# Kernel tuning notes

Hardware: AMD Instinct MI355X
Metric: run time of the kernel (lower is better)

The kernel has to match this reference:

```python
import jax, jax.numpy as jnp
import numpy as np

B, S, T, H, V = 32, 64, 64, 512, 32000


def setup_inputs() -> dict:
    key = jax.random.key(0)
    ks = jax.random.split(key, 16)
    sc = 1.0 / np.sqrt(H)
    return {
        "encoder_outputs": jax.random.normal(ks[0], (B, S, H), jnp.float32),
        "encoder_hidden": jax.random.normal(ks[1], (1, B, H), jnp.float32),
        "target_tensor": jax.random.randint(ks[2], (B, T), 0, V),
        "max_len": T,
        "emb": jax.random.normal(ks[3], (V, H), jnp.float32) * 0.02,
        "Wa_w": jax.random.normal(ks[4], (H, H), jnp.float32) * sc,
        "Wa_b": jnp.zeros((H,), jnp.float32),
        "Ua_w": jax.random.normal(ks[5], (H, H), jnp.float32) * sc,
        "Ua_b": jnp.zeros((H,), jnp.float32),
        "Va_w": jax.random.normal(ks[6], (1, H), jnp.float32) * sc,
        "Va_b": jnp.zeros((1,), jnp.float32),
        "W_ih": jax.random.normal(ks[7], (3 * H, 2 * H), jnp.float32) * sc,
        "W_hh": jax.random.normal(ks[8], (3 * H, H), jnp.float32) * sc,
        "b_ih": jnp.zeros((3 * H,), jnp.float32),
        "b_hh": jnp.zeros((3 * H,), jnp.float32),
        "out_w": jax.random.normal(ks[9], (V, H), jnp.float32) * sc,
        "out_b": jnp.zeros((V,), jnp.float32),
    }


def reference(encoder_outputs, encoder_hidden, target_tensor, max_len,
              emb, Wa_w, Wa_b, Ua_w, Ua_b, Va_w, Va_b,
              W_ih, W_hh, b_ih, b_hh, out_w, out_b):
    # Teacher-forcing decode; dropout in eval mode (identity).
    keys = encoder_outputs                      # [B,S,H]
    Ua_keys = keys @ Ua_w.T + Ua_b              # precompute Ua(keys): same math each step
    bsz = keys.shape[0]
    # token fed at step 0 is SOS (=0), then target_tensor[:, i-1]
    tokens = jnp.concatenate(
        [jnp.zeros((bsz, 1), target_tensor.dtype), target_tensor[:, : max_len - 1]], axis=1
    )  # [B,T]

    def step(h, tok):                            # h: [B,H], tok: [B]
        e = emb[tok]                             # [B,H] embedding gather
        q = h @ Wa_w.T + Wa_b                    # Wa(query)
        s = jnp.tanh(q[:, None, :] + Ua_keys)    # [B,S,H]
        scores = (s @ Va_w.T + Va_b)[..., 0]     # [B,S]
        w = jax.nn.softmax(scores, axis=-1)      # [B,S]
        ctx = jnp.einsum('bs,bsh->bh', w, keys)  # [B,H]
        x = jnp.concatenate([e, ctx], axis=-1)   # [B,2H]
        gi = x @ W_ih.T + b_ih                   # [B,3H]
        gh = h @ W_hh.T + b_hh                   # [B,3H]
        ir, iz, inn = jnp.split(gi, 3, axis=-1)
        hr, hz, hn = jnp.split(gh, 3, axis=-1)
        r = jax.nn.sigmoid(ir + hr)
        z = jax.nn.sigmoid(iz + hz)
        n = jnp.tanh(inn + r * hn)
        h_new = (1.0 - z) * n + z * h            # GRU cell (PyTorch convention)
        logits = h_new @ out_w.T + out_b         # [B,V]
        return h_new, (logits, w)

    h0 = encoder_hidden[0]                       # [B,H]
    hT, (logits, attn) = jax.lax.scan(step, h0, jnp.swapaxes(tokens, 0, 1))
    logits = jnp.swapaxes(logits, 0, 1)          # [B,T,V]
    decoder_outputs = jax.nn.log_softmax(logits, axis=-1)
    attentions = jnp.swapaxes(attn, 0, 1)        # [B,T,S]
    return decoder_outputs, hT[None], attentions
```

## Files before the change

### kernel.cpp

```cpp
#include <hip/hip_runtime.h>
#include <hip/hip_bf16.h>
#include <hip/hip_fp16.h>
#include <math.h>

constexpr int B = 32, S = 64, T = 64, H = 512, V = 32000;
constexpr int G3 = 3 * H;
constexpr int BT = B * T;

constexpr size_t UAK_OFF    = 0;
constexpr size_t GIE_OFF    = 1048576;
constexpr size_t KWTH_OFF   = 4194304;
constexpr size_t WA2T_OFF   = 5767168;
constexpr size_t WHH2T_OFF  = 5898240;
constexpr size_t SCPT_OFF   = 6291456;
constexpr size_t FLG_OFF    = 7340032;
constexpr size_t OWBF_OFF   = 0;
constexpr size_t HALL_OFF   = 8192000;
constexpr size_t STATS_OFF  = 8192000;
constexpr size_t HBF_OFF    = 9256960;
constexpr size_t KEYSH_OFF  = 10000000;
constexpr size_t GEH_OFF    = 10524288;
constexpr size_t UAWH_OFF   = 11048576;
constexpr size_t WLOH_OFF   = 11179648;
constexpr size_t WCTXH_OFF  = 11572864;

typedef __attribute__((ext_vector_type(8))) short bf16x8;
typedef __attribute__((ext_vector_type(4))) float f32x4;
typedef __attribute__((ext_vector_type(4))) int i32x4;
typedef _Float16 f16x8 __attribute__((ext_vector_type(8)));
typedef _Float16 h2v __attribute__((ext_vector_type(2)));

__device__ __forceinline__ float fast_tanh(float x) {
  float ax = fabsf(x);
  float e = __expf(-2.f * ax);
  float r = (1.f - e) / (1.f + e);
  return x < 0.f ? -r : r;
}
__device__ __forceinline__ float fast_sig(float x) {
  return 1.f / (1.f + __expf(-x));
}
__device__ __forceinline__ unsigned pack_h2(float a, float b) {
  __half2 h = __floats2half2_rn(a, b);
  return *(unsigned*)&h;
}
__device__ __forceinline__ ushort f2h(float v) {
  __half h = __float2half(v);
  return *(ushort*)&h;
}
__device__ __forceinline__ void unp2(unsigned v, float* d) {
  __half2 h = *(__half2*)&v;
  d[0] = __low2float(h); d[1] = __high2float(h);
}
__device__ __forceinline__ float dot2acc(unsigned w, unsigned h, float c) {
  return __builtin_amdgcn_fdot2(__builtin_bit_cast(h2v, w),
                                __builtin_bit_cast(h2v, h), c, false);
}
__device__ __forceinline__ int poll8(const int* p) {
  i32x4 a, b;
  asm volatile("global_load_dwordx4 %0, %2, off sc0 sc1\n\t"
               "global_load_dwordx4 %1, %3, off sc0 sc1\n\t"
               "s_waitcnt vmcnt(0)"
               : "=v"(a), "=v"(b) : "v"(p), "v"(p + 4) : "memory");
  return a.x & a.y & a.z & a.w & b.x & b.y & b.z & b.w;
}
__device__ __forceinline__ void store_coh_i32(int* p, int v) {
  asm volatile("global_store_dword %0, %1, off sc0 sc1" :: "v"(p), "v"(v) : "memory");
}
__device__ __forceinline__ void store_coh_f32(float* p, float v) {
  asm volatile("global_store_dword %0, %1, off sc0 sc1" :: "v"(p), "v"(v) : "memory");
}

__global__ void k_prep(const float* __restrict__ eh, const int* __restrict__ tgt,
                       const float* __restrict__ keys, const float* __restrict__ emb,
                       const float* __restrict__ Ua_w, const float* __restrict__ W_ih,
                       const float* __restrict__ Wa_w, const float* __restrict__ W_hh,
                       float* __restrict__ ws) {
  int blk = blockIdx.x, tid = threadIdx.x;
  if (blk < 256) {
    int i = blk * 256 + tid;
    ((int*)(ws + FLG_OFF))[i] = 0;
    if (i < B * H) ws[HALL_OFF + i] = eh[i];
    return;
  }
  if (blk < 1280) {
    int i4 = ((blk - 256) * 256 + tid) * 4;
    float4 v = *(const float4*)&keys[i4];
    ushort4 o; o.x = f2h(v.x); o.y = f2h(v.y); o.z = f2h(v.z); o.w = f2h(v.w);
    *(ushort4*)&((ushort*)(ws + KEYSH_OFF))[i4] = o;
    return;
  }
  if (blk < 2304) {
    int i4 = ((blk - 1280) * 256 + tid) * 4;
    int row = i4 >> 9, k = i4 & 511;
    int tok = (row & 63) ? tgt[row - 1] : 0;
    float4 v = *(const float4*)&emb[(size_t)tok * 512 + k];
    ushort4 o; o.x = f2h(v.x); o.y = f2h(v.y); o.z = f2h(v.z); o.w = f2h(v.w);
    *(ushort4*)&((ushort*)(ws + GEH_OFF))[i4] = o;
    return;
  }
  if (blk < 2560) {
    int i4 = ((blk - 2304) * 256 + tid) * 4;
    float4 v = *(const float4*)&Ua_w[i4];
    ushort4 o; o.x = f2h(v.x); o.y = f2h(v.y); o.z = f2h(v.z); o.w = f2h(v.w);
    *(ushort4*)&((ushort*)(ws + UAWH_OFF))[i4] = o;
    return;
  }
  if (blk < 3328) {
    int i4 = ((blk - 2560) * 256 + tid) * 4;
    int row = i4 >> 9, k = i4 & 511;
    float4 v = *(const float4*)&W_ih[(size_t)row * 1024 + k];
    ushort4 o; o.x = f2h(v.x); o.y = f2h(v.y); o.z = f2h(v.z); o.w = f2h(v.w);
    *(ushort4*)&((ushort*)(ws + WLOH_OFF))[i4] = o;
    return;
  }
  if (blk < 4096) {
    int i4 = ((blk - 3328) * 256 + tid) * 4;
    int row = i4 >> 9, k = i4 & 511;
    float4 v = *(const float4*)&W_ih[(size_t)row * 1024 + 512 + k];
    ushort4 o; o.x = f2h(v.x); o.y = f2h(v.y); o.z = f2h(v.z); o.w = f2h(v.w);
    *(ushort4*)&((ushort*)(ws + WCTXH_OFF))[i4] = o;
    return;
  }
  if (blk < 4608) {
    int i = (blk - 4096) * 256 + tid;
    int r = i >> 8, kk = i & 255;
    float2 v = *(const float2*)&Wa_w[(size_t)r * 512 + 2 * kk];
    ((unsigned*)(ws + WA2T_OFF))[(size_t)kk * 512 + r] = pack_h2(v.x, v.y);
    return;
  }
  {
    int i = (blk - 4608) * 256 + tid;
    int r = i >> 8, kk = i & 255;
    float2 v = *(const float2*)&W_hh[(size_t)r * 512 + 2 * kk];
    ((unsigned*)(ws + WHH2T_OFF))[(size_t)kk * 1536 + r] = pack_h2(v.x, v.y);
  }
}

__global__ void k_conv_outw(const float* __restrict__ w, ushort* __restrict__ o, int n4) {
  int i = blockIdx.x * blockDim.x + threadIdx.x;
  if (i < n4) {
    float4 v = *(const float4*)&w[(size_t)i * 4];
    ushort4 u;
    __hip_bfloat16 h0 = __float2bfloat16(v.x); u.x = *(ushort*)&h0;
    __hip_bfloat16 h1 = __float2bfloat16(v.y); u.y = *(ushort*)&h1;
    __hip_bfloat16 h2 = __float2bfloat16(v.z); u.z = *(ushort*)&h2;
    __hip_bfloat16 h3 = __float2bfloat16(v.w); u.w = *(ushort*)&h3;
    *(ushort4*)&o[(size_t)i * 4] = u;
  }
}

__global__ __launch_bounds__(256) void k_mfma128(
    const ushort* __restrict__ Ah, const ushort* __restrict__ Bh,
    const float* __restrict__ bias, float* __restrict__ C, int ldc) {
  __shared__ __align__(16) ushort As[128 * 32];
  __shared__ __align__(16) ushort Bs[128 * 32];
  int bm = blockIdx.y, bn = blockIdx.x;
  int tid = threadIdx.x;
  int lane = tid & 63, wv = tid >> 6;
  int wm = wv >> 1, wn = wv & 1;
  int kc = lane >> 4, rl = lane & 15;
  f32x4 acc[4][4] = {};
  int c0 = wv * 128 + lane, c1 = c0 + 64;
  const ushort* ga0 = Ah + (size_t)(bm * 128 + (c0 >> 2)) * 512 + (c0 & 3) * 8;
  const ushort* ga1 = Ah + (size_t)(bm * 128 + (c1 >> 2)) * 512 + (c1 & 3) * 8;
  const ushort* gb0 = Bh + (size_t)(bn * 128 + (c0 >> 2)) * 512 + (c0 & 3) * 8;
  const ushort* gb1 = Bh + (size_t)(bn * 128 + (c1 >> 2)) * 512 + (c1 & 3) * 8;
  for (int k0 = 0; k0 < 512; k0 += 32) {
    __syncthreads();
    __builtin_amdgcn_global_load_lds(
        (const __attribute__((address_space(1))) void*)(ga0 + k0),
        (__attribute__((address_space(3))) void*)((char*)As + wv * 2048), 16, 0, 0);
    __builtin_amdgcn_global_load_lds(
        (const __attribute__((address_space(1))) void*)(ga1 + k0),
        (__attribute__((address_space(3))) void*)((char*)As + wv * 2048 + 1024), 16, 0, 0);
    __builtin_amdgcn_global_load_lds(
        (const __attribute__((address_space(1))) void*)(gb0 + k0),
        (__attribute__((address_space(3))) void*)((char*)Bs + wv * 2048), 16, 0, 0);
    __builtin_amdgcn_global_load_lds(
        (const __attribute__((address_space(1))) void*)(gb1 + k0),
        (__attribute__((address_space(3))) void*)((char*)Bs + wv * 2048 + 1024), 16, 0, 0);
    __syncthreads();
    f16x8 af[4], bfv[4];
#pragma unroll
    for (int f = 0; f < 4; f++) {
      af[f] = *(const f16x8*)&As[(wm * 64 + f * 16 + rl) * 32 + kc * 8];
      bfv[f] = *(const f16x8*)&Bs[(wn * 64 + f * 16 + rl) * 32 + kc * 8];
    }
#pragma unroll
    for (int i = 0; i < 4; i++)
#pragma unroll
      for (int j = 0; j < 4; j++)
        acc[i][j] = __builtin_amdgcn_mfma_f32_16x16x32_f16(af[i], bfv[j], acc[i][j], 0, 0, 0);
  }
  int cl = lane & 15, rg = lane >> 4;
#pragma unroll
  for (int i = 0; i < 4; i++) {
    int m = bm * 128 + wm * 64 + i * 16 + rg * 4;
#pragma unroll
    for (int j = 0; j < 4; j++) {
      int n = bn * 128 + wn * 64 + j * 16 + cl;
      float bv = bias[n];
#pragma unroll
      for (int r = 0; r < 4; r++)
        C[(size_t)(m + r) * ldc + n] = acc[i][j][r] + bv;
    }
  }
}

__global__ __launch_bounds__(256) void k_mfma_kwt(
    const ushort* __restrict__ Wctxh, const ushort* __restrict__ keysh,
    ushort* __restrict__ KWTh) {
  __shared__ __align__(16) ushort As[128 * 32];
  __shared__ __align__(16) ushort Bs[64 * 32];
  int bm = blockIdx.x, b = blockIdx.y;
  int tid = threadIdx.x;
  int lane = tid & 63, wv = tid >> 6;
  int kc = lane >> 4, rl = lane & 15;
  f32x4 acc[2][4] = {};
  int c0 = tid, c2 = tid + 256;
  const ushort* ga0 = Wctxh + (size_t)(bm * 128 + (c0 >> 2)) * 512 + (c0 & 3) * 8;
  const ushort* ga1 = Wctxh + (size_t)(bm * 128 + (c2 >> 2)) * 512 + (c2 & 3) * 8;
  const ushort* gb0 = keysh + (size_t)(b * 64 + (c0 >> 2)) * 512 + (c0 & 3) * 8;
  for (int k0 = 0; k0 < 512; k0 += 32) {
    __syncthreads();
    __builtin_amdgcn_global_load_lds(
        (const __attribute__((address_space(1))) void*)(ga0 + k0),
        (__attribute__((address_space(3))) void*)((char*)As + wv * 1024), 16, 0, 0);
    __builtin_amdgcn_global_load_lds(
        (const __attribute__((address_space(1))) void*)(ga1 + k0),
        (__attribute__((address_space(3))) void*)((char*)As + 4096 + wv * 1024), 16, 0, 0);
    __builtin_amdgcn_global_load_lds(
        (const __attribute__((address_space(1))) void*)(gb0 + k0),
        (__attribute__((address_space(3))) void*)((char*)Bs + wv * 1024), 16, 0, 0);
    __syncthreads();
    f16x8 af[2], bfv[4];
#pragma unroll
    for (int f = 0; f < 2; f++)
      af[f] = *(const f16x8*)&As[(wv * 32 + f * 16 + rl) * 32 + kc * 8];
#pragma unroll
    for (int j = 0; j < 4; j++)
      bfv[j] = *(const f16x8*)&Bs[(j * 16 + rl) * 32 + kc * 8];
#pragma unroll
    for (int i = 0; i < 2; i++)
#pragma unroll
      for (int j = 0; j < 4; j++)
        acc[i][j] = __builtin_amdgcn_mfma_f32_16x16x32_f16(af[i], bfv[j], acc[i][j], 0, 0, 0);
  }
  int cl = lane & 15, rg = lane >> 4;
#pragma unroll
  for (int i = 0; i < 2; i++) {
    int m = bm * 128 + wv * 32 + i * 16 + rg * 4;
#pragma unroll
    for (int j = 0; j < 4; j++) {
      int n = j * 16 + cl;
#pragma unroll
      for (int r = 0; r < 4; r++)
        KWTh[((size_t)b * G3 + m + r) * 64 + n] = f2h(acc[i][j][r]);
    }
  }
}

__global__ __launch_bounds__(256) void k_recur(
    const float* __restrict__ Wa_b, const float* __restrict__ Va_w,
    const float* __restrict__ Va_b, const float* __restrict__ b_hh,
    const unsigned* __restrict__ WA2T, const unsigned* __restrict__ WHH2T,
    float* __restrict__ ws, float* __restrict__ attn_out, float* __restrict__ ht_out) {
  const int w = blockIdx.x;
  const int tid = threadIdx.x;
  const int b = w & 31, cb = w >> 5;
  const int j0 = cb * 64;
  int* flg = (int*)(ws + FLG_OFF);
  __hip_bfloat16* HBF = (__hip_bfloat16*)(ws + HBF_OFF);
  const float* GIE = ws + GIE_OFF;
  float* SCPT = ws + SCPT_OFF;
  const ushort* KWTh = (const ushort*)(ws + KWTH_OFF);

  __shared__ float sKWT[192][68];
  __shared__ float sUAK[64][68];
  __shared__ unsigned sH2[256];
  __shared__ float sq[64];
  __shared__ float qp[64][5];
  __shared__ float spp[64][5];
  __shared__ float swt[64];
  __shared__ float sga[4][64];
  __shared__ float sVa[64], sWab[64], sBhh[192];

#pragma unroll
  for (int g = 0; g < 3; g++) {
    int jl = tid >> 2, part = tid & 3;
    const ushort* src = KWTh + ((size_t)b * G3 + g * 512 + j0 + jl) * 64 + part * 16;
    float* dst = &sKWT[g * 64 + jl][part * 16];
    uint4 u0 = *(const uint4*)src;
    uint4 u1 = *(const uint4*)(src + 8);
    unp2(u0.x, dst); unp2(u0.y, dst + 2); unp2(u0.z, dst + 4); unp2(u0.w, dst + 6);
    unp2(u1.x, dst + 8); unp2(u1.y, dst + 10); unp2(u1.z, dst + 12); unp2(u1.w, dst + 14);
  }
  {
    int s = tid >> 2, part = tid & 3;
    const float* src = ws + UAK_OFF + ((size_t)(b * 64 + s)) * 512 + j0 + part * 16;
    float* dst = &sUAK[s][part * 16];
#pragma unroll
    for (int i = 0; i < 16; i += 4) *(float4*)&dst[i] = *(const float4*)&src[i];
  }
  if (tid < 64) { sVa[tid] = Va_w[j0 + tid]; sWab[tid] = Wa_b[j0 + tid]; }
  if (tid < 192) sBhh[tid] = b_hh[(tid >> 6) * 512 + j0 + (tid & 63)];
  const float va_b = Va_b[0];
  __syncthreads();

  for (int t = 0; t < T; ++t) {
    const float* hcur = ws + HALL_OFF + (size_t)t * B * H + b * H;
    float gival = 0.f;
    if (tid < 192)
      gival = GIE[((size_t)b * T + t) * G3 + (tid >> 6) * 512 + j0 + (tid & 63)];
    if (t > 0) {
      if (tid == 0) {
        const int* fb = flg + (size_t)(t - 1) * 1024 + b * 32;
        while (!poll8(fb)) {}
      }
    }
    __syncthreads();
    {
      float2 h2 = *(const float2*)&hcur[2 * tid];
      sH2[tid] = pack_h2(h2.x, h2.y);
    }
    __syncthreads();

    {
      int jq = tid & 63, kp = tid >> 6;
      const unsigned* wp = WA2T + (size_t)(kp * 64) * 512 + j0 + jq;
      float acc = 0.f;
#pragma unroll 8
      for (int kk = 0; kk < 64; kk++)
        acc = dot2acc(wp[(size_t)kk * 512], sH2[kp * 64 + kk], acc);
      qp[jq][kp] = acc;
    }
    __syncthreads();
    if (tid < 64)
      sq[tid] = qp[tid][0] + qp[tid][1] + qp[tid][2] + qp[tid][3] + sWab[tid];
    __syncthreads();
    {
      int s = tid >> 2, jc = tid & 3;
      float accs = 0.f;
#pragma unroll
      for (int i = 0; i < 16; i++) {
        int j = jc * 16 + i;
        accs += sVa[j] * fast_tanh(sq[j] + sUAK[s][j]);
      }
      spp[s][jc] = accs;
    }
    __syncthreads();
    if (tid < 64) {
      float v = spp[tid][0] + spp[tid][1] + spp[tid][2] + spp[tid][3];
      if (cb == 0) v += va_b;
      store_coh_f32(SCPT + (((size_t)t * B + b) * 8 + cb) * 64 + tid, v);
    }
    if (tid == 0) {
      asm volatile("s_waitcnt vmcnt(0)" ::: "memory");
      store_coh_i32(flg + (size_t)t * 1024 + b * 32 + 8 + cb, 1);
    }

    float gh = 0.f;
    if (tid < 192) {
      int gate = tid >> 6, lane = tid & 63;
      const unsigned* wp = WHH2T + gate * 512 + j0 + lane;
      float g0 = 0.f, g1 = 0.f;
#pragma unroll 8
      for (int kk = 0; kk < 256; kk += 2) {
        g0 = dot2acc(wp[(size_t)kk * 1536], sH2[kk], g0);
        g1 = dot2acc(wp[(size_t)(kk + 1) * 1536], sH2[kk + 1], g1);
      }
      gh = g0 + g1 + sBhh[tid];
    }
    if (tid == 0) {
      const int* fs = flg + (size_t)t * 1024 + b * 32 + 8;
      while (!poll8(fs)) {}
    }
    __syncthreads();
    if (tid < 64) {
      const float* sp = SCPT + ((size_t)t * B + b) * 512;
      float v = (sp[tid] + sp[64 + tid]) + (sp[128 + tid] + sp[192 + tid])
              + (sp[256 + tid] + sp[320 + tid]) + (sp[384 + tid] + sp[448 + tid]);
      float m = v;
      for (int o = 32; o; o >>= 1) m = fmaxf(m, __shfl_xor(m, o, 64));
      float e = __expf(v - m);
      float su = e;
      for (int o = 32; o; o >>= 1) su += __shfl_xor(su, o, 64);
      float wt = e / su;
      swt[tid] = wt;
      if (cb == 0) attn_out[((size_t)b * T + t) * S + tid] = wt;
    }
    __syncthreads();
    if (tid < 192) {
      int gate = tid >> 6, lane = tid & 63;
      float gic = 0.f;
#pragma unroll
      for (int s4 = 0; s4 < 64; s4 += 4) {
        float4 k4 = *(const float4*)&sKWT[tid][s4];
        gic += k4.x * swt[s4] + k4.y * swt[s4 + 1] + k4.z * swt[s4 + 2] + k4.w * swt[s4 + 3];
      }
      float gi = gival + gic;
      if (gate == 0) sga[0][lane] = gi + gh;
      else if (gate == 1) sga[1][lane] = gi + gh;
      else { sga[2][lane] = gi; sga[3][lane] = gh; }
    }
    __syncthreads();
    if (tid < 64) {
      float r = fast_sig(sga[0][tid]);
      float z = fast_sig(sga[1][tid]);
      float n = fast_tanh(sga[2][tid] + r * sga[3][tid]);
      float hold = hcur[j0 + tid];
      float hn = (1.f - z) * n + z * hold;
      HBF[((size_t)b * T + t) * H + j0 + tid] = __float2bfloat16(hn);
      if (t < T - 1)
        store_coh_f32(ws + HALL_OFF + (size_t)(t + 1) * B * H + b * H + j0 + tid, hn);
      else
        ht_out[b * H + j0 + tid] = hn;
    }
    if (tid == 0 && t < T - 1) {
      asm volatile("s_waitcnt vmcnt(0)" ::: "memory");
      store_coh_i32(flg + (size_t)t * 1024 + b * 32 + cb, 1);
    }
    __syncthreads();
  }
}

__global__ __launch_bounds__(256) void k_outgemm(
    const __hip_bfloat16* __restrict__ Abf, const __hip_bfloat16* __restrict__ Bbf,
    const float* __restrict__ bias, float* __restrict__ Cmat,
    float* __restrict__ stats) {
  __shared__ __align__(16) short As[128 * 32];
  __shared__ __align__(16) short Bs[128 * 32];
  __shared__ float sredM[2][128];
  __shared__ float sredS[2][128];
  int bm = blockIdx.y, bn = blockIdx.x;
  int tid = threadIdx.x;
  int lane = tid & 63, wv = tid >> 6;
  int wm = wv >> 1, wn = wv & 1;
  int kc = lane >> 4, rl = lane & 15;
  f32x4 acc[4][4] = {};
  int c0 = wv * 128 + lane, c1 = c0 + 64;
  const __hip_bfloat16* ga0 = Abf + (size_t)(bm * 128 + (c0 >> 2)) * 512 + (c0 & 3) * 8;
  const __hip_bfloat16* ga1 = Abf + (size_t)(bm * 128 + (c1 >> 2)) * 512 + (c1 & 3) * 8;
  const __hip_bfloat16* gb0 = Bbf + (size_t)(bn * 128 + (c0 >> 2)) * 512 + (c0 & 3) * 8;
  const __hip_bfloat16* gb1 = Bbf + (size_t)(bn * 128 + (c1 >> 2)) * 512 + (c1 & 3) * 8;
  for (int k0 = 0; k0 < 512; k0 += 32) {
    __syncthreads();
    __builtin_amdgcn_global_load_lds(
        (const __attribute__((address_space(1))) void*)(ga0 + k0),
        (__attribute__((address_space(3))) void*)((char*)As + wv * 2048), 16, 0, 0);
    __builtin_amdgcn_global_load_lds(
        (const __attribute__((address_space(1))) void*)(ga1 + k0),
        (__attribute__((address_space(3))) void*)((char*)As + wv * 2048 + 1024), 16, 0, 0);
    __builtin_amdgcn_global_load_lds(
        (const __attribute__((address_space(1))) void*)(gb0 + k0),
        (__attribute__((address_space(3))) void*)((char*)Bs + wv * 2048), 16, 0, 0);
    __builtin_amdgcn_global_load_lds(
        (const __attribute__((address_space(1))) void*)(gb1 + k0),
        (__attribute__((address_space(3))) void*)((char*)Bs + wv * 2048 + 1024), 16, 0, 0);
    __syncthreads();
    bf16x8 af[4], bfv[4];
#pragma unroll
    for (int f = 0; f < 4; f++) {
      af[f] = *(const bf16x8*)&As[(wm * 64 + f * 16 + rl) * 32 + kc * 8];
      bfv[f] = *(const bf16x8*)&Bs[(wn * 64 + f * 16 + rl) * 32 + kc * 8];
    }
#pragma unroll
    for (int i = 0; i < 4; i++)
#pragma unroll
      for (int j = 0; j < 4; j++)
        acc[i][j] = __builtin_amdgcn_mfma_f32_16x16x32_bf16(af[i], bfv[j], acc[i][j], 0, 0, 0);
  }
  int cl = lane & 15, rg = lane >> 4;
  float bv[4];
#pragma unroll
  for (int j = 0; j < 4; j++) bv[j] = bias[bn * 128 + wn * 64 + j * 16 + cl];
  float vmax[4][4];
#pragma unroll
  for (int i = 0; i < 4; i++) {
    int m = bm * 128 + wm * 64 + i * 16 + rg * 4;
#pragma unroll
    for (int r = 0; r < 4; r++) vmax[i][r] = -1e30f;
#pragma unroll
    for (int j = 0; j < 4; j++) {
      int n = bn * 128 + wn * 64 + j * 16 + cl;
#pragma unroll
      for (int r = 0; r < 4; r++) {
        float val = acc[i][j][r] + bv[j];
        Cmat[(size_t)(m + r) * V + n] = val;
        vmax[i][r] = fmaxf(vmax[i][r], val);
      }
    }
  }
#pragma unroll
  for (int o = 1; o < 16; o <<= 1)
#pragma unroll
    for (int i = 0; i < 4; i++)
#pragma unroll
      for (int r = 0; r < 4; r++)
        vmax[i][r] = fmaxf(vmax[i][r], __shfl_xor(vmax[i][r], o, 64));
  float vsum[4][4] = {};
#pragma unroll
  for (int i = 0; i < 4; i++)
#pragma unroll
    for (int j = 0; j < 4; j++)
#pragma unroll
      for (int r = 0; r < 4; r++)
        vsum[i][r] += __expf(acc[i][j][r] + bv[j] - vmax[i][r]);
#pragma unroll
  for (int o = 1; o < 16; o <<= 1)
#pragma unroll
    for (int i = 0; i < 4; i++)
#pragma unroll
      for (int r = 0; r < 4; r++)
        vsum[i][r] += __shfl_xor(vsum[i][r], o, 64);
  if (cl == 0) {
#pragma unroll
    for (int i = 0; i < 4; i++)
#pragma unroll
      for (int r = 0; r < 4; r++) {
        int rowl = wm * 64 + i * 16 + rg * 4 + r;
        sredM[wn][rowl] = vmax[i][r];
        sredS[wn][rowl] = vsum[i][r];
      }
  }
  __syncthreads();
  if (tid < 128) {
    float m0 = sredM[0][tid], m1 = sredM[1][tid];
    float M = fmaxf(m0, m1);
    float Sv = sredS[0][tid] * __expf(m0 - M) + sredS[1][tid] * __expf(m1 - M);
    float* st = stats + (size_t)(bm * 128 + tid) * 512 + bn * 2;
    st[0] = M; st[1] = Sv;
  }
}

__global__ __launch_bounds__(256) void k_lsm_final(float* __restrict__ Cmat,
                                                   const float* __restrict__ stats) {
  int row = blockIdx.x;
  int tid = threadIdx.x;
  __shared__ float sM[4], sS[4];
  float m = -1e30f, s = 0.f;
  if (tid < 250) {
    float2 v = *(const float2*)&stats[(size_t)row * 512 + tid * 2];
    m = v.x; s = v.y;
  }
  for (int o = 32; o; o >>= 1) {
    float om = __shfl_xor(m, o, 64), os = __shfl_xor(s, o, 64);
    float nm = fmaxf(m, om);
    s = s * __expf(m - nm) + os * __expf(om - nm);
    m = nm;
  }
  if ((tid & 63) == 0) { sM[tid >> 6] = m; sS[tid >> 6] = s; }
  __syncthreads();
  float M = fmaxf(fmaxf(sM[0], sM[1]), fmaxf(sM[2], sM[3]));
  float Ssum = sS[0] * __expf(sM[0] - M) + sS[1] * __expf(sM[1] - M)
             + sS[2] * __expf(sM[2] - M) + sS[3] * __expf(sM[3] - M);
  float lse = M + __logf(Ssum);
  float* p = Cmat + (size_t)row * V;
  for (int i = tid * 4; i < V; i += 1024) {
    float4 v = *(const float4*)&p[i];
    v.x -= lse; v.y -= lse; v.z -= lse; v.w -= lse;
    *(float4*)&p[i] = v;
  }
}

extern "C" void kernel_launch(void* const* d_in, const int* in_sizes, int n_in,
                              void* d_out, int out_size, void* d_ws, size_t ws_size,
                              hipStream_t stream) {
  (void)in_sizes; (void)n_in; (void)out_size; (void)ws_size;
  const float* keys = (const float*)d_in[0];
  const float* ehid = (const float*)d_in[1];
  const int* tgt    = (const int*)d_in[2];
  const float* emb  = (const float*)d_in[4];
  const float* Wa_w = (const float*)d_in[5];
  const float* Wa_b = (const float*)d_in[6];
  const float* Ua_w = (const float*)d_in[7];
  const float* Ua_b = (const float*)d_in[8];
  const float* Va_w = (const float*)d_in[9];
  const float* Va_b = (const float*)d_in[10];
  const float* W_ih = (const float*)d_in[11];
  const float* W_hh = (const float*)d_in[12];
  const float* b_ih = (const float*)d_in[13];
  const float* b_hh = (const float*)d_in[14];
  const float* out_w = (const float*)d_in[15];
  const float* out_b = (const float*)d_in[16];
  float* ws = (float*)d_ws;
  float* out = (float*)d_out;
  float* logits = out;
  float* ht_out = out + (size_t)B * T * V;
  float* attn_out = ht_out + (size_t)B * H;

  hipLaunchKernelGGL(k_prep, dim3(6144), dim3(256), 0, stream,
                     ehid, tgt, keys, emb, Ua_w, W_ih, Wa_w, W_hh, ws);
  hipLaunchKernelGGL(k_mfma128, dim3(4, 16), dim3(256), 0, stream,
                     (const ushort*)(ws + KEYSH_OFF), (const ushort*)(ws + UAWH_OFF),
                     Ua_b, ws + UAK_OFF, 512);
  hipLaunchKernelGGL(k_mfma128, dim3(12, 16), dim3(256), 0, stream,
                     (const ushort*)(ws + GEH_OFF), (const ushort*)(ws + WLOH_OFF),
                     b_ih, ws + GIE_OFF, G3);
  hipLaunchKernelGGL(k_mfma_kwt, dim3(12, 32), dim3(256), 0, stream,
                     (const ushort*)(ws + WCTXH_OFF), (const ushort*)(ws + KEYSH_OFF),
                     (ushort*)(ws + KWTH_OFF));
  hipLaunchKernelGGL(k_recur, dim3(256), dim3(256), 0, stream,
                     Wa_b, Va_w, Va_b, b_hh,
                     (const unsigned*)(ws + WA2T_OFF), (const unsigned*)(ws + WHH2T_OFF),
                     ws, attn_out, ht_out);
  hipLaunchKernelGGL(k_conv_outw, dim3((V * H / 4 + 255) / 256), dim3(256), 0, stream,
                     out_w, (ushort*)(ws + OWBF_OFF), V * H / 4);
  hipLaunchKernelGGL(k_outgemm, dim3(250, 16), dim3(256), 0, stream,
                     (const __hip_bfloat16*)(ws + HBF_OFF),
                     (const __hip_bfloat16*)(ws + OWBF_OFF), out_b, logits,
                     ws + STATS_OFF);
  hipLaunchKernelGGL(k_lsm_final, dim3(BT), dim3(256), 0, stream,
                     logits, ws + STATS_OFF);
}
```

Measured before the change: 956.4 us.

## Add L2-local fast-path flags to recurrence sync and swizzle outgemm block order

Each recurrence barrier now writes a duplicate flag with a plain store. Waiters first poll that copy with an sc0-only load, which can hit in L2 when producer and consumer share an XCD, and fall back to the system-coherent flags otherwise. This is meant to cut spin-wait latency across the 64 serial steps, at the cost of extra flag stores and a doubled poll loop. Separately, the output GEMM grid is padded to 256 columns and its column blocks are remapped in interleaved groups of 8. The intent is to improve L2 locality of output-weight tiles across XCDs, while 6 padding blocks per row exit early.

```diff
diff --git a/kernel.cpp b/kernel.cpp
--- a/kernel.cpp
+++ b/kernel.cpp
@@ -55,7 +55,7 @@
   return __builtin_amdgcn_fdot2(__builtin_bit_cast(h2v, w),
                                 __builtin_bit_cast(h2v, h), c, false);
 }
-__device__ __forceinline__ int poll8(const int* p) {
+__device__ __forceinline__ int poll8_coh(const int* p) {
   i32x4 a, b;
   asm volatile("global_load_dwordx4 %0, %2, off sc0 sc1\n\t"
                "global_load_dwordx4 %1, %3, off sc0 sc1\n\t"
@@ -63,8 +63,19 @@
                : "=v"(a), "=v"(b) : "v"(p), "v"(p + 4) : "memory");
   return a.x & a.y & a.z & a.w & b.x & b.y & b.z & b.w;
 }
+__device__ __forceinline__ int poll8_l2(const int* p) {
+  i32x4 a, b;
+  asm volatile("global_load_dwordx4 %0, %2, off sc0\n\t"
+               "global_load_dwordx4 %1, %3, off sc0\n\t"
+               "s_waitcnt vmcnt(0)"
+               : "=v"(a), "=v"(b) : "v"(p), "v"(p + 4) : "memory");
+  return a.x & a.y & a.z & a.w & b.x & b.y & b.z & b.w;
+}
 __device__ __forceinline__ void store_coh_i32(int* p, int v) {
   asm volatile("global_store_dword %0, %1, off sc0 sc1" :: "v"(p), "v"(v) : "memory");
+}
+__device__ __forceinline__ void store_plain_i32(int* p, int v) {
+  asm volatile("global_store_dword %0, %1, off" :: "v"(p), "v"(v) : "memory");
 }
 __device__ __forceinline__ void store_coh_f32(float* p, float v) {
   asm volatile("global_store_dword %0, %1, off sc0 sc1" :: "v"(p), "v"(v) : "memory");
@@ -314,8 +325,12 @@
       gival = GIE[((size_t)b * T + t) * G3 + (tid >> 6) * 512 + j0 + (tid & 63)];
     if (t > 0) {
       if (tid == 0) {
-        const int* fb = flg + (size_t)(t - 1) * 1024 + b * 32;
-        while (!poll8(fb)) {}
+        const int* fF = flg + (size_t)(t - 1) * 1024 + b * 32 + 16;
+        const int* fS = flg + (size_t)(t - 1) * 1024 + b * 32;
+        while (true) {
+          if (poll8_l2(fF)) break;
+          if (poll8_coh(fS)) break;
+        }
       }
     }
     __syncthreads();
@@ -356,6 +371,7 @@
     }
     if (tid == 0) {
       asm volatile("s_waitcnt vmcnt(0)" ::: "memory");
+      store_plain_i32(flg + (size_t)t * 1024 + b * 32 + 24 + cb, 1);
       store_coh_i32(flg + (size_t)t * 1024 + b * 32 + 8 + cb, 1);
     }
 
@@ -372,8 +388,12 @@
       gh = g0 + g1 + sBhh[tid];
     }
     if (tid == 0) {
-      const int* fs = flg + (size_t)t * 1024 + b * 32 + 8;
-      while (!poll8(fs)) {}
+      const int* fF = flg + (size_t)t * 1024 + b * 32 + 24;
+      const int* fS = flg + (size_t)t * 1024 + b * 32 + 8;
+      while (true) {
+        if (poll8_l2(fF)) break;
+        if (poll8_coh(fS)) break;
+      }
     }
     __syncthreads();
     if (tid < 64) {
@@ -418,6 +438,7 @@
     }
     if (tid == 0 && t < T - 1) {
       asm volatile("s_waitcnt vmcnt(0)" ::: "memory");
+      store_plain_i32(flg + (size_t)t * 1024 + b * 32 + 16 + cb, 1);
       store_coh_i32(flg + (size_t)t * 1024 + b * 32 + cb, 1);
     }
     __syncthreads();
@@ -432,7 +453,10 @@
   __shared__ __align__(16) short Bs[128 * 32];
   __shared__ float sredM[2][128];
   __shared__ float sredS[2][128];
-  int bm = blockIdx.y, bn = blockIdx.x;
+  int xv = blockIdx.x;
+  int bn = (xv & 7) * 32 + (xv >> 3);
+  if (bn >= 250) return;
+  int bm = blockIdx.y;
   int tid = threadIdx.x;
   int lane = tid & 63, wv = tid >> 6;
   int wm = wv >> 1, wn = wv & 1;
@@ -606,7 +630,7 @@
                      ws, attn_out, ht_out);
   hipLaunchKernelGGL(k_conv_outw, dim3((V * H / 4 + 255) / 256), dim3(256), 0, stream,
                      out_w, (ushort*)(ws + OWBF_OFF), V * H / 4);
-  hipLaunchKernelGGL(k_outgemm, dim3(250, 16), dim3(256), 0, stream,
+  hipLaunchKernelGGL(k_outgemm, dim3(256, 16), dim3(256), 0, stream,
                      (const __hip_bfloat16*)(ws + HBF_OFF),
                      (const __hip_bfloat16*)(ws + OWBF_OFF), out_b, logits,
                      ws + STATS_OFF);
```

Measured after the change: 939.3 us (median of 2 runs). No clear change (-1.8%).

## Restructure recurrent step to one grid sync per step with redundant attention scores

Applied to the files above, without the earlier changes.

Each of the 8 column-blocks per batch now computes its slice of the next step's Wa query projection right after its GRU update and publishes the partials to a double-buffered global array. Every block reduces the eight partials and computes the full 64x512 attention score tile locally from an fp16 Ua-keys copy in LDS. This removes the second cross-block flag wait and score exchange each step, at the cost of redundant tanh work and more LDS. The context-gate product now uses packed fp16 dot2, and the output GEMM's block index is remapped to group column tiles, with padded grid blocks returning early.

```diff
diff --git a/kernel.cpp b/kernel.cpp
--- a/kernel.cpp
+++ b/kernel.cpp
@@ -12,7 +12,7 @@
 constexpr size_t KWTH_OFF   = 4194304;
 constexpr size_t WA2T_OFF   = 5767168;
 constexpr size_t WHH2T_OFF  = 5898240;
-constexpr size_t SCPT_OFF   = 6291456;
+constexpr size_t QP_OFF     = 6291456;
 constexpr size_t FLG_OFF    = 7340032;
 constexpr size_t OWBF_OFF   = 0;
 constexpr size_t HALL_OFF   = 8192000;
@@ -47,10 +47,6 @@
   __half h = __float2half(v);
   return *(ushort*)&h;
 }
-__device__ __forceinline__ void unp2(unsigned v, float* d) {
-  __half2 h = *(__half2*)&v;
-  d[0] = __low2float(h); d[1] = __high2float(h);
-}
 __device__ __forceinline__ float dot2acc(unsigned w, unsigned h, float c) {
   return __builtin_amdgcn_fdot2(__builtin_bit_cast(h2v, w),
                                 __builtin_bit_cast(h2v, h), c, false);
@@ -68,6 +64,11 @@
 }
 __device__ __forceinline__ void store_coh_f32(float* p, float v) {
   asm volatile("global_store_dword %0, %1, off sc0 sc1" :: "v"(p), "v"(v) : "memory");
+}
+__device__ __forceinline__ float load_coh_f32(const float* p) {
+  float v;
+  asm volatile("global_load_dword %0, %1, off sc0 sc1" : "=v"(v) : "v"(p) : "memory");
+  return v;
 }
 
 __global__ void k_prep(const float* __restrict__ eh, const int* __restrict__ tgt,
@@ -78,7 +79,7 @@
   int blk = blockIdx.x, tid = threadIdx.x;
   if (blk < 256) {
     int i = blk * 256 + tid;
-    ((int*)(ws + FLG_OFF))[i] = 0;
+    if (i < T * B * 8) ((int*)(ws + FLG_OFF))[i] = 0;
     if (i < B * H) ws[HALL_OFF + i] = eh[i];
     return;
   }
@@ -272,93 +273,85 @@
   int* flg = (int*)(ws + FLG_OFF);
   __hip_bfloat16* HBF = (__hip_bfloat16*)(ws + HBF_OFF);
   const float* GIE = ws + GIE_OFF;
-  float* SCPT = ws + SCPT_OFF;
-  const ushort* KWTh = (const ushort*)(ws + KWTH_OFF);
-
-  __shared__ float sKWT[192][68];
-  __shared__ float sUAK[64][68];
+  float* QP = ws + QP_OFF;
+  const unsigned* KWT32 = (const unsigned*)(ws + KWTH_OFF);
+
+  __shared__ unsigned sUA[64][261];
+  __shared__ unsigned sKW[192][37];
   __shared__ unsigned sH2[256];
-  __shared__ float sq[64];
-  __shared__ float qp[64][5];
+  __shared__ unsigned sHn2[32];
+  __shared__ float sq[512];
+  __shared__ float sVa[512], sWab[512];
   __shared__ float spp[64][5];
   __shared__ float swt[64];
+  __shared__ unsigned sW2[32];
   __shared__ float sga[4][64];
-  __shared__ float sVa[64], sWab[64], sBhh[192];
-
-#pragma unroll
-  for (int g = 0; g < 3; g++) {
-    int jl = tid >> 2, part = tid & 3;
-    const ushort* src = KWTh + ((size_t)b * G3 + g * 512 + j0 + jl) * 64 + part * 16;
-    float* dst = &sKWT[g * 64 + jl][part * 16];
-    uint4 u0 = *(const uint4*)src;
-    uint4 u1 = *(const uint4*)(src + 8);
-    unp2(u0.x, dst); unp2(u0.y, dst + 2); unp2(u0.z, dst + 4); unp2(u0.w, dst + 6);
-    unp2(u1.x, dst + 8); unp2(u1.y, dst + 10); unp2(u1.z, dst + 12); unp2(u1.w, dst + 14);
-  }
-  {
-    int s = tid >> 2, part = tid & 3;
-    const float* src = ws + UAK_OFF + ((size_t)(b * 64 + s)) * 512 + j0 + part * 16;
-    float* dst = &sUAK[s][part * 16];
-#pragma unroll
-    for (int i = 0; i < 16; i += 4) *(float4*)&dst[i] = *(const float4*)&src[i];
-  }
-  if (tid < 64) { sVa[tid] = Va_w[j0 + tid]; sWab[tid] = Wa_b[j0 + tid]; }
+  __shared__ float shn[64];
+  __shared__ float sBhh[192];
+
+  for (int idx = tid; idx < 64 * 256; idx += 256) {
+    int s = idx >> 8, jp = idx & 255;
+    float2 u = *(const float2*)&ws[UAK_OFF + ((size_t)(b * 64 + s)) * 512 + 2 * jp];
+    sUA[s][jp] = pack_h2(u.x, u.y);
+  }
+  for (int idx = tid; idx < 192 * 32; idx += 256) {
+    int row = idx >> 5, sp = idx & 31;
+    int col = (row >> 6) * 512 + j0 + (row & 63);
+    sKW[row][sp] = KWT32[((size_t)b * G3 + col) * 32 + sp];
+  }
+  sVa[tid] = Va_w[tid];   sVa[tid + 256] = Va_w[tid + 256];
+  sWab[tid] = Wa_b[tid];  sWab[tid + 256] = Wa_b[tid + 256];
   if (tid < 192) sBhh[tid] = b_hh[(tid >> 6) * 512 + j0 + (tid & 63)];
   const float va_b = Va_b[0];
+  if (tid < 64) shn[tid] = ws[HALL_OFF + (size_t)b * H + j0 + tid];
+  if (tid < 32) sHn2[tid] = pack_h2(shn[2 * tid], shn[2 * tid + 1]);
   __syncthreads();
+  {
+    const unsigned* wp = WA2T + (size_t)(cb * 32) * 512;
+    float a = 0.f, c = 0.f;
+#pragma unroll 8
+    for (int kk = 0; kk < 32; kk++) {
+      unsigned hp = sHn2[kk];
+      a = dot2acc(wp[(size_t)kk * 512 + tid], hp, a);
+      c = dot2acc(wp[(size_t)kk * 512 + tid + 256], hp, c);
+    }
+    float* qd = QP + ((size_t)b * 8 + cb) * 512;
+    store_coh_f32(qd + tid, a);
+    store_coh_f32(qd + tid + 256, c);
+  }
+  asm volatile("s_waitcnt vmcnt(0)" ::: "memory");
+  __syncthreads();
+  if (tid == 0) store_coh_i32(&flg[((size_t)b) * 8 + cb], 1);
 
   for (int t = 0; t < T; ++t) {
     const float* hcur = ws + HALL_OFF + (size_t)t * B * H + b * H;
     float gival = 0.f;
     if (tid < 192)
       gival = GIE[((size_t)b * T + t) * G3 + (tid >> 6) * 512 + j0 + (tid & 63)];
-    if (t > 0) {
-      if (tid == 0) {
-        const int* fb = flg + (size_t)(t - 1) * 1024 + b * 32;
-        while (!poll8(fb)) {}
-      }
+    if (tid == 0) {
+      const int* f = flg + ((size_t)t * B + b) * 8;
+      while (!poll8(f)) {}
     }
     __syncthreads();
     {
       float2 h2 = *(const float2*)&hcur[2 * tid];
       sH2[tid] = pack_h2(h2.x, h2.y);
     }
-    __syncthreads();
-
     {
-      int jq = tid & 63, kp = tid >> 6;
-      const unsigned* wp = WA2T + (size_t)(kp * 64) * 512 + j0 + jq;
-      float acc = 0.f;
-#pragma unroll 8
-      for (int kk = 0; kk < 64; kk++)
-        acc = dot2acc(wp[(size_t)kk * 512], sH2[kp * 64 + kk], acc);
-      qp[jq][kp] = acc;
-    }
-    __syncthreads();
-    if (tid < 64)
-      sq[tid] = qp[tid][0] + qp[tid][1] + qp[tid][2] + qp[tid][3] + sWab[tid];
-    __syncthreads();
-    {
-      int s = tid >> 2, jc = tid & 3;
-      float accs = 0.f;
-#pragma unroll
-      for (int i = 0; i < 16; i++) {
-        int j = jc * 16 + i;
-        accs += sVa[j] * fast_tanh(sq[j] + sUAK[s][j]);
-      }
-      spp[s][jc] = accs;
-    }
-    __syncthreads();
-    if (tid < 64) {
-      float v = spp[tid][0] + spp[tid][1] + spp[tid][2] + spp[tid][3];
-      if (cb == 0) v += va_b;
-      store_coh_f32(SCPT + (((size_t)t * B + b) * 8 + cb) * 64 + tid, v);
-    }
-    if (tid == 0) {
+      const float* qb = QP + ((size_t)(t & 1) * B + b) * 8 * 512;
+      float va[8], vc[8];
+#pragma unroll
+      for (int i = 0; i < 8; i++) va[i] = load_coh_f32(qb + i * 512 + tid);
+#pragma unroll
+      for (int i = 0; i < 8; i++) vc[i] = load_coh_f32(qb + i * 512 + tid + 256);
       asm volatile("s_waitcnt vmcnt(0)" ::: "memory");
-      store_coh_i32(flg + (size_t)t * 1024 + b * 32 + 8 + cb, 1);
-    }
-
+      __builtin_amdgcn_sched_barrier(0);
+      float a0 = ((va[0] + va[1]) + (va[2] + va[3])) + ((va[4] + va[5]) + (va[6] + va[7]));
+      float a1 = ((vc[0] + vc[1]) + (vc[2] + vc[3])) + ((vc[4] + vc[5]) + (vc[6] + vc[7]));
+      sq[tid] = a0 + sWab[tid];
+      sq[tid + 256] = a1 + sWab[tid + 256];
+    }
+    __syncthreads();
     float gh = 0.f;
     if (tid < 192) {
       int gate = tid >> 6, lane = tid & 63;
@@ -371,15 +364,24 @@
       }
       gh = g0 + g1 + sBhh[tid];
     }
-    if (tid == 0) {
-      const int* fs = flg + (size_t)t * 1024 + b * 32 + 8;
-      while (!poll8(fs)) {}
+    {
+      int s = tid & 63, jr = tid >> 6;
+      const unsigned* ur = &sUA[s][jr * 64];
+      const float* qq = sq + jr * 128;
+      const float* vv = sVa + jr * 128;
+      float a0 = 0.f, a1 = 0.f;
+#pragma unroll 4
+      for (int i = 0; i < 64; i++) {
+        unsigned u = ur[i];
+        __half2 hu = *(__half2*)&u;
+        a0 += vv[2 * i] * fast_tanh(qq[2 * i] + __low2float(hu));
+        a1 += vv[2 * i + 1] * fast_tanh(qq[2 * i + 1] + __high2float(hu));
+      }
+      spp[s][jr] = a0 + a1;
     }
     __syncthreads();
     if (tid < 64) {
-      const float* sp = SCPT + ((size_t)t * B + b) * 512;
-      float v = (sp[tid] + sp[64 + tid]) + (sp[128 + tid] + sp[192 + tid])
-              + (sp[256 + tid] + sp[320 + tid]) + (sp[384 + tid] + sp[448 + tid]);
+      float v = spp[tid][0] + spp[tid][1] + spp[tid][2] + spp[tid][3] + va_b;
       float m = v;
       for (int o = 32; o; o >>= 1) m = fmaxf(m, __shfl_xor(m, o, 64));
       float e = __expf(v - m);
@@ -388,17 +390,20 @@
       float wt = e / su;
       swt[tid] = wt;
       if (cb == 0) attn_out[((size_t)b * T + t) * S + tid] = wt;
+      float w0 = __shfl(wt, 2 * (tid & 31), 64);
+      float w1 = __shfl(wt, 2 * (tid & 31) + 1, 64);
+      if (tid < 32) sW2[tid] = pack_h2(w0, w1);
     }
     __syncthreads();
     if (tid < 192) {
       int gate = tid >> 6, lane = tid & 63;
-      float gic = 0.f;
-#pragma unroll
-      for (int s4 = 0; s4 < 64; s4 += 4) {
-        float4 k4 = *(const float4*)&sKWT[tid][s4];
-        gic += k4.x * swt[s4] + k4.y * swt[s4 + 1] + k4.z * swt[s4 + 2] + k4.w * swt[s4 + 3];
+      float c0 = 0.f, c1 = 0.f;
+#pragma unroll 8
+      for (int sp = 0; sp < 32; sp += 2) {
+        c0 = dot2acc(sKW[tid][sp], sW2[sp], c0);
+        c1 = dot2acc(sKW[tid][sp + 1], sW2[sp + 1], c1);
       }
-      float gi = gival + gic;
+      float gi = gival + c0 + c1;
       if (gate == 0) sga[0][lane] = gi + gh;
       else if (gate == 1) sga[1][lane] = gi + gh;
       else { sga[2][lane] = gi; sga[3][lane] = gh; }
@@ -411,16 +416,31 @@
       float hold = hcur[j0 + tid];
       float hn = (1.f - z) * n + z * hold;
       HBF[((size_t)b * T + t) * H + j0 + tid] = __float2bfloat16(hn);
+      shn[tid] = hn;
       if (t < T - 1)
         store_coh_f32(ws + HALL_OFF + (size_t)(t + 1) * B * H + b * H + j0 + tid, hn);
       else
         ht_out[b * H + j0 + tid] = hn;
     }
-    if (tid == 0 && t < T - 1) {
-      asm volatile("s_waitcnt vmcnt(0)" ::: "memory");
-      store_coh_i32(flg + (size_t)t * 1024 + b * 32 + cb, 1);
-    }
-    __syncthreads();
+    if (tid < 32) sHn2[tid] = pack_h2(shn[2 * tid], shn[2 * tid + 1]);
+    __syncthreads();
+    if (t < T - 1) {
+      const unsigned* wp = WA2T + (size_t)(cb * 32) * 512;
+      float a = 0.f, c = 0.f;
+#pragma unroll 8
+      for (int kk = 0; kk < 32; kk++) {
+        unsigned hp = sHn2[kk];
+        a = dot2acc(wp[(size_t)kk * 512 + tid], hp, a);
+        c = dot2acc(wp[(size_t)kk * 512 + tid + 256], hp, c);
+      }
+      float* qd = QP + (((size_t)((t + 1) & 1) * B + b) * 8 + cb) * 512;
+      store_coh_f32(qd + tid, a);
+      store_coh_f32(qd + tid + 256, c);
+    }
+    asm volatile("s_waitcnt vmcnt(0)" ::: "memory");
+    __syncthreads();
+    if (tid == 0 && t < T - 1)
+      store_coh_i32(&flg[((size_t)(t + 1) * B + b) * 8 + cb], 1);
   }
 }
 
@@ -432,7 +452,10 @@
   __shared__ __align__(16) short Bs[128 * 32];
   __shared__ float sredM[2][128];
   __shared__ float sredS[2][128];
-  int bm = blockIdx.y, bn = blockIdx.x;
+  int xv = blockIdx.x;
+  int bn = (xv & 7) * 32 + (xv >> 3);
+  if (bn >= 250) return;
+  int bm = blockIdx.y;
   int tid = threadIdx.x;
   int lane = tid & 63, wv = tid >> 6;
   int wm = wv >> 1, wn = wv & 1;
@@ -606,7 +629,7 @@
                      ws, attn_out, ht_out);
   hipLaunchKernelGGL(k_conv_outw, dim3((V * H / 4 + 255) / 256), dim3(256), 0, stream,
                      out_w, (ushort*)(ws + OWBF_OFF), V * H / 4);
-  hipLaunchKernelGGL(k_outgemm, dim3(250, 16), dim3(256), 0, stream,
+  hipLaunchKernelGGL(k_outgemm, dim3(256, 16), dim3(256), 0, stream,
                      (const __hip_bfloat16*)(ws + HBF_OFF),
                      (const __hip_bfloat16*)(ws + OWBF_OFF), out_b, logits,
                      ws + STATS_OFF);
```

Result: slower. 1.255 ms (+31.2%).
